# Performance work log

Measured on AMD Instinct MI355X. Metric: run time of the kernel, lower is better.

Reference implementation:

```python
import jax, jax.numpy as jnp
import numpy as np

NUM_HEADS = 8
HEAD_DIM = 128
NUM_HIDDEN = 2048  # memory slots per head
D_MODEL = 1024
B, S = 1, 4096
EPS = 1e-6


def _normalize(kq):
    ss = jnp.sum(jnp.square(kq), axis=-1, keepdims=True)
    return kq * jax.lax.rsqrt(ss + EPS)


def setup_inputs() -> dict:
    key = jax.random.key(0)
    ks = jax.random.split(key, 5)
    x = jax.random.normal(ks[0], (B, S, D_MODEL), dtype=jnp.float32)
    # variance_scaling fan_in ~ stddev 1/sqrt(fan_in); plain normal is fine for a baseline
    Wq = jax.random.normal(ks[1], (D_MODEL, NUM_HEADS * HEAD_DIM), dtype=jnp.float32) / np.sqrt(D_MODEL)
    keys = jax.random.normal(ks[2], (NUM_HIDDEN * NUM_HEADS, HEAD_DIM), dtype=jnp.float32)
    values = jax.random.normal(ks[3], (NUM_HIDDEN * NUM_HEADS, HEAD_DIM), dtype=jnp.float32)
    attn_scale = jnp.ones((NUM_HEADS,), dtype=jnp.float32)
    Wo = jax.random.normal(ks[4], (NUM_HEADS * HEAD_DIM, D_MODEL), dtype=jnp.float32) / np.sqrt(NUM_HEADS * HEAD_DIM)
    return {"x": x, "Wq": Wq, "keys": keys, "values": values, "attn_scale": attn_scale, "Wo": Wo}


def reference(x, Wq, keys, values, attn_scale, Wo):
    # reshape memory bank: (k*h, d) -> (k, h, d)
    k = keys.reshape(NUM_HIDDEN, NUM_HEADS, HEAD_DIM)
    v = values.reshape(NUM_HIDDEN, NUM_HEADS, HEAD_DIM)
    # query projection, split heads: [B,S,h*d] -> [B,S,h,d]
    q = jnp.einsum('bsm,mn->bsn', x, Wq).reshape(B, S, NUM_HEADS, HEAD_DIM)
    # L2-normalize keys and queries; fold learned per-head scale into keys
    k = _normalize(k) * attn_scale.reshape(1, NUM_HEADS, 1)
    q = _normalize(q)
    # attention against fixed memory bank: [B,S,h,k]
    attn = jnp.einsum('bshd,khd->bshk', q, k)
    attn = jax.nn.softmax(attn, axis=-1)
    # read values: [B,S,h,d] -> merge heads -> output projection
    y = jnp.einsum('bshk,khd->bshd', attn, v).reshape(B, S, NUM_HEADS * HEAD_DIM)
    return jnp.einsum('bsn,no->bso', y, Wo)
```

## Files before the change

### kernel.cpp

```cpp
#include <hip/hip_runtime.h>
#include <math.h>

#define S_LEN 4096
#define DM 1024
#define NHEADS 8
#define HDIM 128
#define NSLOTS 2048

typedef __attribute__((ext_vector_type(8))) short bf16x8;
typedef __attribute__((ext_vector_type(4))) float f32x4;
typedef __attribute__((ext_vector_type(16))) float f32x16;
typedef __attribute__((ext_vector_type(4))) unsigned u32x4;

static __device__ __forceinline__ unsigned short f2bf(float f) {
  union { float f; unsigned u; } v; v.f = f;
  unsigned u = v.u;
  return (unsigned short)((u + 0x7fffu + ((u >> 16) & 1u)) >> 16);
}
static __device__ __forceinline__ unsigned pack2(float a, float b) {
  return (unsigned)f2bf(a) | ((unsigned)f2bf(b) << 16);
}
static __device__ __forceinline__ f32x4 mfma16(bf16x8 a, bf16x8 b, f32x4 c) {
  return __builtin_amdgcn_mfma_f32_16x16x32_bf16(a, b, c, 0, 0, 0);
}
static __device__ __forceinline__ f32x16 mfma32(bf16x8 a, bf16x8 b, f32x16 c) {
  return __builtin_amdgcn_mfma_f32_32x32x16_bf16(a, b, c, 0, 0, 0);
}
static __device__ __forceinline__ void gll16(const void* g, void* l) {
  __builtin_amdgcn_global_load_lds(
      (__attribute__((address_space(1))) void*)(void*)(unsigned long long)(const char*)g,
      (__attribute__((address_space(3))) void*)l, 16, 0, 0);
}
static __device__ __forceinline__ float fexp2(float x) {
  float r;
  asm("v_exp_f32 %0, %1" : "=v"(r) : "v"(x));
  return r;
}


__global__ __launch_bounds__(256) void prep_kernel(
    const float* __restrict__ x, const float* __restrict__ Wq,
    const float* __restrict__ Wo, const float* __restrict__ keys,
    const float* __restrict__ values, const float* __restrict__ scale,
    unsigned short* __restrict__ xb, unsigned short* __restrict__ wqt,
    unsigned short* __restrict__ wot, unsigned* __restrict__ kbf_w,
    unsigned short* __restrict__ vt) {
  __shared__ float tileU[64 * 129];
  int b = blockIdx.x, t = threadIdx.x;

  if (b < 1024) {
    int mb = b >> 4, kb64 = b & 15;
#pragma unroll
    for (int p = 0; p < 4; p++) {
      int fi = t + 256 * p;
      int row = fi >> 4, kq = fi & 15;
      float4 v = *(const float4*)(x + ((size_t)(mb * 64 + row) * DM + kb64 * 64 + kq * 4));
      float* d = &tileU[row * 65 + kq * 4];
      d[0] = v.x; d[1] = v.y; d[2] = v.z; d[3] = v.w;
    }
    __syncthreads();
#pragma unroll
    for (int p2 = 0; p2 < 2; p2++) {
      int g = t + 256 * p2;
      int kb = g >> 6, row = g & 63;
      const float* src = &tileU[row * 65 + kb * 8];
      u32x4 w;
#pragma unroll
      for (int q = 0; q < 4; q++) w[q] = pack2(src[2 * q], src[2 * q + 1]);
      *(u32x4*)(xb + ((size_t)(mb * 16 + kb64) * 8 + kb) * 512 + row * 8) = w;
    }
  } else if (b < 1280) {
    int b2 = b - 1024;
    const float* W = (b2 < 128) ? Wq : Wo;
    unsigned short* WT = (b2 < 128) ? wqt : wot;
    int r = b2 & 127;
    int nb = r >> 4, kb64 = r & 15;
#pragma unroll
    for (int p = 0; p < 8; p++) {
      int fi = t + 256 * p;
      int krow = fi >> 5, nq = fi & 31;
      float4 v = *(const float4*)(W + ((size_t)(kb64 * 64 + krow) * DM + nb * 128 + nq * 4));
      float* d = &tileU[krow * 129 + nq * 4];
      d[0] = v.x; d[1] = v.y; d[2] = v.z; d[3] = v.w;
    }
    __syncthreads();
#pragma unroll
    for (int p2 = 0; p2 < 4; p2++) {
      int g = t + 256 * p2;
      int pp = g >> 6, r6 = g & 63;
      int kb = pp >> 1, rh = pp & 1;
      u32x4 w;
#pragma unroll
      for (int q = 0; q < 4; q++)
        w[q] = pack2(tileU[(kb * 8 + 2 * q) * 129 + rh * 64 + r6],
                     tileU[(kb * 8 + 2 * q + 1) * 129 + rh * 64 + r6]);
      *(u32x4*)(WT + ((size_t)(nb * 16 + kb64) * 16 + pp) * 512 + r6 * 8) = w;
    }
  } else if (b < 5376) {
    int b3 = b - 1280;
    int w = b3 * 4 + (t >> 6);
    int lane = t & 63;
    int slot = w >> 3, h = w & 7;
    float2 v = ((const float2*)(keys + (size_t)w * HDIM))[lane];
    float ss = v.x * v.x + v.y * v.y;
#pragma unroll
    for (int m = 1; m < 64; m <<= 1) ss += __shfl_xor(ss, m);
    float sc = scale[h] * rsqrtf(ss + 1e-6f);
    size_t off = (size_t)h * 131072 + (slot >> 6) * 4096 +
                 (((slot >> 5) & 1) * 8 + (lane >> 3)) * 256 + ((lane >> 2) & 1) * 128 +
                 (slot & 31) * 4 + (lane & 3);
    kbf_w[off] = pack2(v.x * sc, v.y * sc);
  } else {
    int b4 = b - 5376;
    int h = b4 >> 5, c = b4 & 31;
#pragma unroll
    for (int p = 0; p < 8; p++) {
      int fi = t + 256 * p;
      int srow = fi >> 5, dq = fi & 31;
      float4 v = *(const float4*)(values +
                                  ((size_t)((c * 64 + srow) * NHEADS + h) * HDIM + dq * 4));
      float* d = &tileU[srow * 129 + dq * 4];
      d[0] = v.x; d[1] = v.y; d[2] = v.z; d[3] = v.w;
    }
    __syncthreads();
#pragma unroll
    for (int p2 = 0; p2 < 4; p2++) {
      int g = t + 256 * p2;
      int sb = g >> 7, d = g & 127;
      u32x4 w;
#pragma unroll
      for (int q = 0; q < 4; q++)
        w[q] = pack2(tileU[(sb * 8 + 2 * q) * 129 + d], tileU[(sb * 8 + 2 * q + 1) * 129 + d]);
      *(u32x4*)(vt + (size_t)h * 262144 + c * 8192 + (sb * 128 + d) * 8) = w;
    }
  }
}

template <bool FUSE_QNORM>
__global__ __launch_bounds__(256) void gemm_nt_kernel(const unsigned short* __restrict__ A,
                                                      const unsigned short* __restrict__ Bt,
                                                      float* __restrict__ Cf,
                                                      unsigned short* __restrict__ Cq,
                                                      int M, int N, int K) {
  __shared__ __align__(16) unsigned short As2[2][4096];
  __shared__ __align__(16) unsigned short Bs2[2][8192];
  __shared__ float ssq[64][2];
  int t = threadIdx.x;
  int wave = t >> 6, lane = t & 63;
  int l16 = lane & 15, quad = lane >> 4;
  int m_blk = blockIdx.y * 64, n_blk = blockIdx.x * 128;
  int wm = (wave & 1) * 32, wn = (wave >> 1) * 64;
  int nk64 = K >> 6;
  f32x4 zero = {0.f, 0.f, 0.f, 0.f};
  f32x4 acc[2][4];
#pragma unroll
  for (int i = 0; i < 2; i++)
#pragma unroll
    for (int j = 0; j < 4; j++) acc[i][j] = zero;

  auto stage = [&](int k0, int b) {
    int kb64 = k0 >> 6;
    const unsigned short* Abase = A + ((size_t)(blockIdx.y * nk64 + kb64)) * 4096;
    const unsigned short* Bbase = Bt + ((size_t)(blockIdx.x * nk64 + kb64)) * 8192;
#pragma unroll
    for (int i = 0; i < 2; i++) {
      int kb = wave * 2 + i;
      gll16(Abase + kb * 512 + lane * 8, &As2[b][kb * 512]);
    }
#pragma unroll
    for (int i = 0; i < 4; i++) {
      int j = wave * 4 + i;
      gll16(Bbase + j * 512 + lane * 8, &Bs2[b][j * 512]);
    }
  };

  stage(0, 0);
  for (int k0 = 0; k0 < K; k0 += 64) {
    int b = (k0 >> 6) & 1;
    __syncthreads();
    if (k0 + 64 < K) stage(k0 + 64, b ^ 1);
#pragma unroll
    for (int kk = 0; kk < 2; kk++) {
      bf16x8 af[2], bfr[4];
#pragma unroll
      for (int mt = 0; mt < 2; mt++)
        af[mt] = *(const bf16x8*)&As2[b][((kk * 4 + quad) * 64 + wm + mt * 16 + l16) * 8];
#pragma unroll
      for (int nt = 0; nt < 4; nt++)
        bfr[nt] = *(const bf16x8*)&Bs2[b][((kk * 4 + quad) * 128 + wn + nt * 16 + l16) * 8];
#pragma unroll
      for (int mt = 0; mt < 2; mt++)
#pragma unroll
        for (int nt = 0; nt < 4; nt++) acc[mt][nt] = mfma16(af[mt], bfr[nt], acc[mt][nt]);
    }
  }

  if (FUSE_QNORM) {
#pragma unroll
    for (int mt = 0; mt < 2; mt++)
#pragma unroll
      for (int r = 0; r < 4; r++) {
        float s = 0.f;
#pragma unroll
        for (int nt = 0; nt < 4; nt++) s += acc[mt][nt][r] * acc[mt][nt][r];
#pragma unroll
        for (int d = 1; d < 16; d <<= 1) s += __shfl_xor(s, d);
        if (l16 == 0) ssq[wm + mt * 16 + quad * 4 + r][wave >> 1] = s;
      }
    __syncthreads();
#pragma unroll
    for (int mt = 0; mt < 2; mt++)
#pragma unroll
      for (int r = 0; r < 4; r++) {
        int row = wm + mt * 16 + quad * 4 + r;
        float rs = rsqrtf(ssq[row][0] + ssq[row][1] + 1e-6f) * 1.44269504f;
#pragma unroll
        for (int nt = 0; nt < 4; nt++)
          Cq[(size_t)(m_blk + row) * N + n_blk + wn + nt * 16 + l16] =
              f2bf(acc[mt][nt][r] * rs);
      }
  } else {
#pragma unroll
    for (int mt = 0; mt < 2; mt++)
#pragma unroll
      for (int nt = 0; nt < 4; nt++)
#pragma unroll
        for (int r = 0; r < 4; r++)
          Cf[(size_t)(m_blk + wm + mt * 16 + quad * 4 + r) * N + n_blk + wn + nt * 16 +
             l16] = acc[mt][nt][r];
  }
}

__global__ __launch_bounds__(256, 2) void attn_kernel(const unsigned short* __restrict__ qbf,
                                                      const unsigned short* __restrict__ kbf,
                                                      const unsigned short* __restrict__ vt,
                                                      const float* __restrict__ scale,
                                                      unsigned short* __restrict__ yb) {
  __shared__ __align__(16) char smem[43008];
  unsigned short(*Ks)[8192] = (unsigned short(*)[8192])smem;
  unsigned short(*pbuf)[32][40] = (unsigned short(*)[32][40])(smem + 32768);
  int h = blockIdx.x, t = threadIdx.x;
  int wave = t >> 6, lane = t & 63;
  int l32 = lane & 31, h8 = lane >> 5;
  int g = wave >> 1, s = wave & 1;
  int q0 = blockIdx.y * 64 + g * 32;
  const unsigned short* Kh = kbf + (size_t)h * 262144;
  const unsigned short* Vh = vt + (size_t)h * 262144;
  float M2 = fabsf(scale[h]) * 1.44269504f;

  bf16x8 aq[8];
  const unsigned short* qrow = qbf + (size_t)(q0 + l32) * DM + h * HDIM + h8 * 8;
#pragma unroll
  for (int dt = 0; dt < 8; dt++) aq[dt] = *(const bf16x8*)(qrow + dt * 16);

  f32x16 zero16 = {};
  f32x16 O[4];
#pragma unroll
  for (int i = 0; i < 4; i++) O[i] = zero16;
  float lsum[16];
#pragma unroll
  for (int r = 0; r < 16; r++) lsum[r] = 0.f;

  auto stage = [&](int c, int b) {
#pragma unroll
    for (int ii = 0; ii < 4; ii++) {
      int j = wave * 4 + ii;
      gll16(Kh + (size_t)c * 8192 + j * 512 + lane * 8, &Ks[b][j * 512]);
    }
  };
  auto loadV = [&](bf16x8(&V)[8], int c) {
#pragma unroll
    for (int nt = 0; nt < 4; nt++)
#pragma unroll
      for (int ks = 0; ks < 2; ks++)
        V[nt * 2 + ks] = *(const bf16x8*)(Vh + (size_t)c * 8192 +
                                          ((s * 4 + ks * 2 + h8) * 128 + nt * 32 + l32) * 8);
  };
  auto body = [&](const unsigned short* Kbuf, bf16x8(&V)[8]) {
    f32x16 acc0 = zero16, acc1 = zero16;
#pragma unroll
    for (int dt = 0; dt < 4; dt++) {
      bf16x8 k0 = *(const bf16x8*)&Kbuf[s * 4096 + ((4 * dt + h8) * 32 + l32) * 8];
      bf16x8 k1 = *(const bf16x8*)&Kbuf[s * 4096 + ((4 * dt + 2 + h8) * 32 + l32) * 8];
      acc0 = mfma32(aq[2 * dt], k0, acc0);
      acc1 = mfma32(aq[2 * dt + 1], k1, acc1);
    }
    f32x16 acc = acc0 + acc1;
#pragma unroll
    for (int r = 0; r < 16; r++) {
      float p = fexp2(acc[r] - M2);
      lsum[r] += p;
      pbuf[wave][(r & 3) + 8 * (r >> 2) + 4 * h8][l32] = f2bf(p);
    }
    bf16x8 pa[2];
#pragma unroll
    for (int ks = 0; ks < 2; ks++)
      pa[ks] = *(const bf16x8*)&pbuf[wave][l32][ks * 16 + h8 * 8];
#pragma unroll
    for (int nt = 0; nt < 4; nt++) {
      f32x16 o = O[nt];
      o = mfma32(pa[0], V[nt * 2 + 0], o);
      o = mfma32(pa[1], V[nt * 2 + 1], o);
      O[nt] = o;
    }
  };

  bf16x8 Vreg0[8], Vreg1[8];
  constexpr int NC = NSLOTS / 64;
  stage(0, 0);
  loadV(Vreg0, 0);
  for (int cc = 0; cc < NC; cc += 2) {
    __syncthreads();
    if (cc + 1 < NC) {
      stage(cc + 1, 1);
      loadV(Vreg1, cc + 1);
    }
    body(&Ks[0][0], Vreg0);
    __syncthreads();
    if (cc + 2 < NC) {
      stage(cc + 2, 0);
      loadV(Vreg0, cc + 2);
    }
    body(&Ks[1][0], Vreg1);
  }

  __syncthreads();
  float(*Oc)[32][128] = (float(*)[32][128])smem;
  float(*Lc)[32][32] = (float(*)[32][32])(smem + 32768);
  if (s == 1) {
#pragma unroll
    for (int nt = 0; nt < 4; nt++)
#pragma unroll
      for (int r = 0; r < 16; r++)
        Oc[g][(r & 3) + 8 * (r >> 2) + 4 * h8][nt * 32 + l32] = O[nt][r];
#pragma unroll
    for (int r = 0; r < 16; r++) Lc[g][(r & 3) + 8 * (r >> 2) + 4 * h8][l32] = lsum[r];
  }
  __syncthreads();
  if (s == 0) {
#pragma unroll
    for (int r = 0; r < 16; r++) {
      int row = (r & 3) + 8 * (r >> 2) + 4 * h8;
      float sum = lsum[r] + Lc[g][row][l32];
#pragma unroll
      for (int d = 1; d < 32; d <<= 1) sum += __shfl_xor(sum, d);
      float inv = 1.0f / sum;
#pragma unroll
      for (int nt = 0; nt < 4; nt++) {
        float v = O[nt][r] + Oc[g][row][nt * 32 + l32];
        size_t off = ((size_t)blockIdx.y * 16 + h * 2 + (nt >> 1)) * 4096 +
                     ((nt & 1) * 4 + (l32 >> 3)) * 512 + (g * 32 + row) * 8 + (l32 & 7);
        yb[off] = f2bf(v * inv);
      }
    }
  }
}


extern "C" void kernel_launch(void* const* d_in, const int* in_sizes, int n_in,
                              void* d_out, int out_size, void* d_ws, size_t ws_size,
                              hipStream_t stream) {
  const float* x = (const float*)d_in[0];
  const float* Wq = (const float*)d_in[1];
  const float* keys = (const float*)d_in[2];
  const float* values = (const float*)d_in[3];
  const float* attn_scale = (const float*)d_in[4];
  const float* Wo = (const float*)d_in[5];
  float* out = (float*)d_out;

  char* ws = (char*)d_ws;
  unsigned short* xb = (unsigned short*)(ws);
  unsigned short* wqt = (unsigned short*)(ws + (8ull << 20));
  unsigned short* wot = (unsigned short*)(ws + (10ull << 20));
  unsigned short* kbf = (unsigned short*)(ws + (12ull << 20));
  unsigned short* vt = (unsigned short*)(ws + (16ull << 20));
  unsigned short* qbf = (unsigned short*)(ws + (20ull << 20));
  unsigned short* yb = (unsigned short*)(ws + (28ull << 20));

  prep_kernel<<<5632, 256, 0, stream>>>(x, Wq, Wo, keys, values, attn_scale, xb, wqt, wot,
                                        (unsigned*)kbf, vt);
  gemm_nt_kernel<true><<<dim3(8, 64), 256, 0, stream>>>(xb, wqt, nullptr, qbf,
                                                        S_LEN, DM, DM);
  attn_kernel<<<dim3(8, 64), 256, 0, stream>>>(qbf, kbf, vt, attn_scale, yb);
  gemm_nt_kernel<false><<<dim3(8, 64), 256, 0, stream>>>(yb, wot, out, nullptr,
                                                         S_LEN, DM, DM);
}
```

Before: 181.1 us.

## Stage V tiles through LDS instead of register double-buffering

Replaces the per-wave register double-buffer of V fragments with a single shared-memory V tile. The tile is loaded with async global-to-LDS copies in the same iteration it is consumed, and an extra barrier sits before the P·V MFMAs. This frees many vector registers and makes V loads coalesced block-wide. In exchange, V load latency is no longer prefetched a chunk ahead and only overlaps the QK and softmax work. It also adds a barrier per chunk and 16KB more LDS per block.

```diff
diff --git a/kernel.cpp b/kernel.cpp
--- a/kernel.cpp
+++ b/kernel.cpp
@@ -236,9 +236,10 @@
                                                       const unsigned short* __restrict__ vt,
                                                       const float* __restrict__ scale,
                                                       unsigned short* __restrict__ yb) {
-  __shared__ __align__(16) char smem[43008];
+  __shared__ __align__(16) char smem[59392];
   unsigned short(*Ks)[8192] = (unsigned short(*)[8192])smem;
-  unsigned short(*pbuf)[32][40] = (unsigned short(*)[32][40])(smem + 32768);
+  unsigned short* Vs = (unsigned short*)(smem + 32768);
+  unsigned short(*pbuf)[32][40] = (unsigned short(*)[32][40])(smem + 49152);
   int h = blockIdx.x, t = threadIdx.x;
   int wave = t >> 6, lane = t & 63;
   int l32 = lane & 31, h8 = lane >> 5;
@@ -261,27 +262,34 @@
 #pragma unroll
   for (int r = 0; r < 16; r++) lsum[r] = 0.f;
 
-  auto stage = [&](int c, int b) {
+  auto stageK = [&](int c, int b) {
 #pragma unroll
     for (int ii = 0; ii < 4; ii++) {
       int j = wave * 4 + ii;
       gll16(Kh + (size_t)c * 8192 + j * 512 + lane * 8, &Ks[b][j * 512]);
     }
   };
-  auto loadV = [&](bf16x8(&V)[8], int c) {
-#pragma unroll
-    for (int nt = 0; nt < 4; nt++)
-#pragma unroll
-      for (int ks = 0; ks < 2; ks++)
-        V[nt * 2 + ks] = *(const bf16x8*)(Vh + (size_t)c * 8192 +
-                                          ((s * 4 + ks * 2 + h8) * 128 + nt * 32 + l32) * 8);
+  auto stageV = [&](int c) {
+#pragma unroll
+    for (int ii = 0; ii < 4; ii++) {
+      int j = wave * 4 + ii;
+      gll16(Vh + (size_t)c * 8192 + j * 512 + lane * 8, &Vs[j * 512]);
+    }
   };
-  auto body = [&](const unsigned short* Kbuf, bf16x8(&V)[8]) {
+
+  constexpr int NC = NSLOTS / 64;
+  stageK(0, 0);
+  for (int c = 0; c < NC; c++) {
+    int b = c & 1;
+    __syncthreads();
+    if (c + 1 < NC) stageK(c + 1, b ^ 1);
+    stageV(c);
+
     f32x16 acc0 = zero16, acc1 = zero16;
 #pragma unroll
     for (int dt = 0; dt < 4; dt++) {
-      bf16x8 k0 = *(const bf16x8*)&Kbuf[s * 4096 + ((4 * dt + h8) * 32 + l32) * 8];
-      bf16x8 k1 = *(const bf16x8*)&Kbuf[s * 4096 + ((4 * dt + 2 + h8) * 32 + l32) * 8];
+      bf16x8 k0 = *(const bf16x8*)&Ks[b][s * 4096 + ((4 * dt + h8) * 32 + l32) * 8];
+      bf16x8 k1 = *(const bf16x8*)&Ks[b][s * 4096 + ((4 * dt + 2 + h8) * 32 + l32) * 8];
       acc0 = mfma32(aq[2 * dt], k0, acc0);
       acc1 = mfma32(aq[2 * dt + 1], k1, acc1);
     }
@@ -296,32 +304,15 @@
 #pragma unroll
     for (int ks = 0; ks < 2; ks++)
       pa[ks] = *(const bf16x8*)&pbuf[wave][l32][ks * 16 + h8 * 8];
+
+    __syncthreads();
 #pragma unroll
     for (int nt = 0; nt < 4; nt++) {
       f32x16 o = O[nt];
-      o = mfma32(pa[0], V[nt * 2 + 0], o);
-      o = mfma32(pa[1], V[nt * 2 + 1], o);
+      o = mfma32(pa[0], *(const bf16x8*)&Vs[((s * 4 + 0 + h8) * 128 + nt * 32 + l32) * 8], o);
+      o = mfma32(pa[1], *(const bf16x8*)&Vs[((s * 4 + 2 + h8) * 128 + nt * 32 + l32) * 8], o);
       O[nt] = o;
     }
-  };
-
-  bf16x8 Vreg0[8], Vreg1[8];
-  constexpr int NC = NSLOTS / 64;
-  stage(0, 0);
-  loadV(Vreg0, 0);
-  for (int cc = 0; cc < NC; cc += 2) {
-    __syncthreads();
-    if (cc + 1 < NC) {
-      stage(cc + 1, 1);
-      loadV(Vreg1, cc + 1);
-    }
-    body(&Ks[0][0], Vreg0);
-    __syncthreads();
-    if (cc + 2 < NC) {
-      stage(cc + 2, 0);
-      loadV(Vreg0, cc + 2);
-    }
-    body(&Ks[1][0], Vreg1);
   }
 
   __syncthreads();
```

Result: no change. 184.1 us (+1.7%).
